# Performance work log

Measured on AMD Instinct MI355X. Metric: run time of the kernel, lower is better.

## Reference

```python
import jax, jax.numpy as jnp
import numpy as np

B = 131072
D = 64          # d_model
T = 4           # num_tiles
TEMP = 0.5


def setup_inputs() -> dict:
    key = jax.random.key(0)
    ks = jax.random.split(key, 16)
    s = 0.02
    return {
        "a_vec": jax.random.normal(ks[0], (B, D), dtype=jnp.float32),
        "b_vec": jax.random.normal(ks[1], (B, D), dtype=jnp.float32),
        "pos_encoding": jax.random.normal(ks[2], (B, 8), dtype=jnp.float32),
        # router: Linear(2D+8 -> D), GELU, Linear(D -> T)
        "Wr1": jax.random.normal(ks[3], (2 * D + 8, D), dtype=jnp.float32) * s,
        "br1": jnp.zeros((D,), dtype=jnp.float32),
        "Wr2": jax.random.normal(ks[4], (D, T), dtype=jnp.float32) * s,
        "br2": jnp.zeros((T,), dtype=jnp.float32),
        # tile nets: per-tile Linear(2D -> 2D), GELU, Linear(2D -> D)
        "W1": jax.random.normal(ks[5], (T, 2 * D, 2 * D), dtype=jnp.float32) * s,
        "b1": jnp.zeros((T, 2 * D), dtype=jnp.float32),
        "W2": jax.random.normal(ks[6], (T, 2 * D, D), dtype=jnp.float32) * s,
        "b2": jnp.zeros((T, D), dtype=jnp.float32),
    }


def _router(x, Wr1, br1, Wr2, br2):
    h = jax.nn.gelu(x @ Wr1 + br1, approximate=False)  # torch nn.GELU is exact
    return (h @ Wr2 + br2) / TEMP


def reference(a_vec, b_vec, pos_encoding, Wr1, br1, Wr2, br2, W1, b1, W2, b2):
    pair = jnp.concatenate([a_vec, b_vec], axis=-1)            # (B, 2D)

    # Routing 1 uses pair; routing 2 uses flipped pair. Both expert passes
    # consume `pair` (faithful to the original code, which feeds pair both times).
    idx1 = jnp.argmax(_router(jnp.concatenate([pair, pos_encoding], -1),
                              Wr1, br1, Wr2, br2), axis=-1)    # (B,)
    pair_flip = jnp.concatenate([b_vec, a_vec], axis=-1)
    idx2 = jnp.argmax(_router(jnp.concatenate([pair_flip, pos_encoding], -1),
                              Wr1, br1, Wr2, br2), axis=-1)    # (B,)

    # Run all tiles on every sample (small T), then gather the routed output.
    h = jax.nn.gelu(jnp.einsum('bi,tij->btj', pair, W1) + b1, approximate=False)  # (B,T,2D)
    out_all = jnp.einsum('bth,thd->btd', h, W2) + b2                              # (B,T,D)

    out1 = jnp.take_along_axis(out_all, idx1[:, None, None], axis=1)[:, 0]
    out2 = jnp.take_along_axis(out_all, idx2[:, None, None], axis=1)[:, 0]
    return out1, out2
```

## Files before the change

kernel.cpp:

```cpp
#include <hip/hip_runtime.h>

#define B_N 131072

using bfrag_t = __attribute__((ext_vector_type(8))) short;
using acc_t   = __attribute__((ext_vector_type(4))) float;
using v4f     = __attribute__((ext_vector_type(4))) float;
using i32x4_t = __attribute__((ext_vector_type(4))) int;

__device__ __forceinline__ unsigned short f2bf(float f) {
  unsigned int u = __float_as_uint(f);
  u += 0x7FFFu + ((u >> 16) & 1u);
  return (unsigned short)(u >> 16);
}

__device__ __forceinline__ unsigned int pk2bf(float x, float y) {
  return (unsigned int)f2bf(x) | ((unsigned int)f2bf(y) << 16);
}

__device__ __forceinline__ void gload_lds16(const void* g, void* l) {
  __builtin_amdgcn_global_load_lds((const __attribute__((address_space(1))) void*)g,
                                   (__attribute__((address_space(3))) void*)l, 16, 0, 0);
}

__device__ __forceinline__ float gelu_f(float x) {
  float ax = fabsf(x) * 0.70710678118654752f;
  float t  = __builtin_amdgcn_rcpf(fmaf(0.3275911f, ax, 1.0f));
  float p  = fmaf(1.061405429f, t, -1.453152027f);
  p = fmaf(p, t, 1.421413741f);
  p = fmaf(p, t, -0.284496736f);
  p = fmaf(p, t, 0.254829592f);
  p = p * t;
  float e  = __expf(-ax * ax);
  float er = fmaf(-p, e, 1.0f);
  er = (x < 0.0f) ? -er : er;
  return 0.5f * x * (1.0f + er);
}

__global__ __launch_bounds__(256) void prepack2_k(
    const float* __restrict__ Wr1, const float* __restrict__ br1,
    const float* __restrict__ Wr2, const float* __restrict__ br2,
    const float* __restrict__ W1, const float* __restrict__ W2,
    float* __restrict__ RW, short* __restrict__ W1s, short* __restrict__ W2s) {
  int gt = blockIdx.x * 256 + threadIdx.x;
  for (int idx = gt; idx < 142 * 64; idx += 16384) {
    int row = idx >> 6, j = idx & 63; float val;
    if (row < 136)      val = Wr1[row * 64 + j];
    else if (row == 136) val = br1[j];
    else if (row < 141) val = Wr2[(row - 137) * 64 + j];
    else                val = (j < 4) ? br2[j] : 0.0f;
    RW[idx] = val;
  }
  for (int ch = gt; ch < 8192; ch += 16384) {
    int t = ch >> 11, r = (ch >> 4) & 127, c = ch & 15;
    const float* src = W1 + t * 16384 + r;
    short* dst = W1s + (t * 128 + r) * 128 + ((c ^ (r & 15)) * 8);
    #pragma unroll
    for (int m = 0; m < 8; m++) dst[m] = (short)f2bf(src[(c * 8 + m) * 128]);
  }
  for (int ch = gt; ch < 4096; ch += 16384) {
    int t = ch >> 10, d = (ch >> 4) & 63, c = ch & 15;
    const float* src = W2 + t * 8192 + d;
    short* dst = W2s + (t * 64 + d) * 128 + ((c ^ (d & 15)) * 8);
    #pragma unroll
    for (int m = 0; m < 8; m++) dst[m] = (short)f2bf(src[(c * 8 + m) * 64]);
  }
}

__global__ __launch_bounds__(256) void router6_k(
    const float* __restrict__ a, const float* __restrict__ b,
    const float* __restrict__ pos, const float* __restrict__ RW,
    unsigned char* __restrict__ r1, unsigned char* __restrict__ r2) {
  __shared__ float SB[17928];
  const int XA = 9088, XB = 13248, PP = 17408;
  int tid = threadIdx.x, wave = tid >> 6, lane = tid & 63;
  int s0 = blockIdx.x * 64;

  for (int it = 0; it < 9; it++) {
    int cb = it * 256 + wave * 64;
    if (cb < 2272) {
      int chunk = cb + lane;
      if (chunk < 2272) gload_lds16(RW + chunk * 4, (char*)SB + cb * 16);
    }
  }
  #pragma unroll
  for (int it = 0; it < 4; it++) {
    int idx = it * 256 + tid;
    int s = idx >> 4, c = idx & 15;
    v4f va = *(const v4f*)(a + (size_t)(s0 + s) * 64 + c * 4);
    v4f vb = *(const v4f*)(b + (size_t)(s0 + s) * 64 + c * 4);
    #pragma unroll
    for (int k = 0; k < 4; k++) {
      SB[XA + (c * 4 + k) * 65 + s] = va[k];
      SB[XB + (c * 4 + k) * 65 + s] = vb[k];
    }
  }
  #pragma unroll
  for (int r = 0; r < 2; r++) {
    int idx = r * 256 + tid;
    int s = idx >> 3, c = idx & 7;
    SB[PP + c * 65 + s] = pos[(size_t)(s0 + s) * 8 + c];
  }
  __syncthreads();

  int sq = tid >> 2, jq = tid & 3;
  v4f acc1[4], acc2[4];
  #pragma unroll
  for (int e = 0; e < 4; e++) {
    v4f bi = *(const v4f*)(SB + 136 * 64 + jq * 16 + e * 4);
    acc1[e] = bi; acc2[e] = bi;
  }
  #pragma unroll 4
  for (int i = 0; i < 64; ++i) {
    float xa = SB[XA + i * 65 + sq];
    float xb = SB[XB + i * 65 + sq];
    const v4f* w = (const v4f*)(SB + i * 64 + jq * 16);
    v4f xav = {xa, xa, xa, xa}, xbv = {xb, xb, xb, xb};
    #pragma unroll
    for (int e = 0; e < 4; e++) {
      v4f wv = w[e];
      acc1[e] = __builtin_elementwise_fma(xav, wv, acc1[e]);
      acc2[e] = __builtin_elementwise_fma(xbv, wv, acc2[e]);
    }
  }
  #pragma unroll 4
  for (int i = 0; i < 64; ++i) {
    float xa = SB[XA + i * 65 + sq];
    float xb = SB[XB + i * 65 + sq];
    const v4f* w = (const v4f*)(SB + (64 + i) * 64 + jq * 16);
    v4f xav = {xa, xa, xa, xa}, xbv = {xb, xb, xb, xb};
    #pragma unroll
    for (int e = 0; e < 4; e++) {
      v4f wv = w[e];
      acc1[e] = __builtin_elementwise_fma(xbv, wv, acc1[e]);
      acc2[e] = __builtin_elementwise_fma(xav, wv, acc2[e]);
    }
  }
  #pragma unroll 2
  for (int i = 0; i < 8; ++i) {
    float p = SB[PP + i * 65 + sq];
    const v4f* w = (const v4f*)(SB + (128 + i) * 64 + jq * 16);
    v4f pv = {p, p, p, p};
    #pragma unroll
    for (int e = 0; e < 4; e++) {
      v4f wv = w[e];
      acc1[e] = __builtin_elementwise_fma(pv, wv, acc1[e]);
      acc2[e] = __builtin_elementwise_fma(pv, wv, acc2[e]);
    }
  }
  #pragma unroll
  for (int e = 0; e < 4; e++) {
    #pragma unroll
    for (int c = 0; c < 4; c++) {
      acc1[e][c] = gelu_f(acc1[e][c]);
      acc2[e][c] = gelu_f(acc2[e][c]);
    }
  }
  __syncthreads();
  #pragma unroll
  for (int e = 0; e < 4; e++) {
    #pragma unroll
    for (int c = 0; c < 4; c++) {
      int j = jq * 16 + e * 4 + c;
      SB[XA + j * 65 + sq] = acc1[e][c];
      SB[XB + j * 65 + sq] = acc2[e][c];
    }
  }
  __syncthreads();
  v4f l1 = *(const v4f*)(SB + 141 * 64);
  v4f l2 = l1;
  #pragma unroll 4
  for (int j = 0; j < 64; ++j) {
    float h1 = SB[XA + j * 65 + sq];
    float h2 = SB[XB + j * 65 + sq];
    v4f w2 = *(const v4f*)(SB + 137 * 64 + j * 4);
    v4f h1v = {h1, h1, h1, h1}, h2v = {h2, h2, h2, h2};
    l1 = __builtin_elementwise_fma(h1v, w2, l1);
    l2 = __builtin_elementwise_fma(h2v, w2, l2);
  }
  int idx1 = 0; float b1v = l1[0];
  if (l1[1] > b1v) { b1v = l1[1]; idx1 = 1; }
  if (l1[2] > b1v) { b1v = l1[2]; idx1 = 2; }
  if (l1[3] > b1v) { b1v = l1[3]; idx1 = 3; }
  int idx2 = 0; float b2v = l2[0];
  if (l2[1] > b2v) { b2v = l2[1]; idx2 = 1; }
  if (l2[2] > b2v) { b2v = l2[2]; idx2 = 2; }
  if (l2[3] > b2v) { b2v = l2[3]; idx2 = 3; }
  if (jq == 0) {
    r1[s0 + sq] = (unsigned char)idx1;
    r2[s0 + sq] = (unsigned char)idx2;
  }
}

__global__ __launch_bounds__(256) void expert2_k(
    const float* __restrict__ a, const float* __restrict__ b,
    const short* __restrict__ W1s, const short* __restrict__ W2s,
    const float* __restrict__ b1, const float* __restrict__ b2,
    const unsigned char* __restrict__ r1, const unsigned char* __restrict__ r2,
    float* __restrict__ out) {
  __shared__ short LB[24576];
  int tid = threadIdx.x;
  int wave = tid >> 6, lane = tid & 63;
  int q = lane >> 4, sm = lane & 15;
  int s0 = blockIdx.x * 128;

  #pragma unroll
  for (int r = 0; r < 8; r++) {
    int slot = r * 256 + tid;
    int g = slot >> 10, sg = slot & 1023;
    int f = sg >> 6, l = sg & 63;
    int sgrp = f >> 2, kb = f & 3;
    int s = s0 + g * 64 + sgrp * 16 + (l & 15);
    int k = kb * 32 + (l >> 4) * 8;
    const float* src = (k < 64) ? (a + s * 64 + k) : (b + s * 64 + (k - 64));
    acc_t v0 = *(const acc_t*)(src);
    acc_t v1 = *(const acc_t*)(src + 4);
    i32x4_t pk;
    pk[0] = (int)pk2bf(v0[0], v0[1]);
    pk[1] = (int)pk2bf(v0[2], v0[3]);
    pk[2] = (int)pk2bf(v1[0], v1[1]);
    pk[3] = (int)pk2bf(v1[2], v1[3]);
    *(i32x4_t*)(&LB[slot * 8]) = pk;
  }
  __syncthreads();
  bfrag_t bfrag[2][4];
  #pragma unroll
  for (int g = 0; g < 2; g++)
    #pragma unroll
    for (int kb = 0; kb < 4; kb++)
      bfrag[g][kb] = *(const bfrag_t*)(&LB[((g * 16 + wave * 4 + kb) * 64 + lane) * 8]);

  int sA = s0 + wave * 16 + sm, sB = sA + 64;
  int i1A = (int)r1[sA], i2A = (int)r2[sA];
  int i1B = (int)r1[sB], i2B = (int)r2[sB];
  __syncthreads();

  acc_t zero = {0.f, 0.f, 0.f, 0.f};
  acc_t o1[2][4], o2[2][4];
  #pragma unroll
  for (int g = 0; g < 2; g++)
    #pragma unroll
    for (int i = 0; i < 4; i++) { o1[g][i] = zero; o2[g][i] = zero; }

  int vb[4];
  #pragma unroll
  for (int kb = 0; kb < 4; kb++) vb[kb] = sm * 256 + (((kb * 4 + q) ^ sm) * 16);
  int addr0 = (((q & 1) * 2) * 16 + sm) * 4;
  int addr1 = addr0 + 64;
  bool hi = (q >> 1) != 0;

  for (int t = 0; t < 4; t++) {
    #pragma unroll
    for (int it = 0; it < 12; it++) {
      int cb = it * 256 + wave * 64;
      int chunk = cb + lane;
      const short* gsrc = (chunk < 2048) ? (W1s + t * 16384 + chunk * 8)
                                         : (W2s + t * 8192 + (chunk - 2048) * 8);
      gload_lds16(gsrc, (char*)LB + cb * 16);
    }
    __syncthreads();
    #pragma unroll
    for (int g = 0; g < 2; g++) {
      unsigned int hp[8][2];
      #pragma unroll
      for (int mt = 0; mt < 8; mt++) {
        acc_t c = zero;
        #pragma unroll
        for (int kb = 0; kb < 4; kb++) {
          bfrag_t A = *(const bfrag_t*)((const char*)LB + mt * 4096 + vb[kb]);
          c = __builtin_amdgcn_mfma_f32_16x16x32_bf16(A, bfrag[g][kb], c, 0, 0, 0);
        }
        acc_t bv = *(const acc_t*)(b1 + t * 128 + mt * 16 + q * 4);
        float g0 = gelu_f(c[0] + bv[0]);
        float g1 = gelu_f(c[1] + bv[1]);
        float g2 = gelu_f(c[2] + bv[2]);
        float g3 = gelu_f(c[3] + bv[3]);
        hp[mt][0] = pk2bf(g0, g1);
        hp[mt][1] = pk2bf(g2, g3);
      }
      bfrag_t b2f[4];
      #pragma unroll
      for (int kb2 = 0; kb2 < 4; kb2++) {
        int p00 = __builtin_amdgcn_ds_bpermute(addr0, (int)hp[2 * kb2][0]);
        int p01 = __builtin_amdgcn_ds_bpermute(addr0, (int)hp[2 * kb2][1]);
        int p10 = __builtin_amdgcn_ds_bpermute(addr1, (int)hp[2 * kb2][0]);
        int p11 = __builtin_amdgcn_ds_bpermute(addr1, (int)hp[2 * kb2][1]);
        int q00 = __builtin_amdgcn_ds_bpermute(addr0, (int)hp[2 * kb2 + 1][0]);
        int q01 = __builtin_amdgcn_ds_bpermute(addr0, (int)hp[2 * kb2 + 1][1]);
        int q10 = __builtin_amdgcn_ds_bpermute(addr1, (int)hp[2 * kb2 + 1][0]);
        int q11 = __builtin_amdgcn_ds_bpermute(addr1, (int)hp[2 * kb2 + 1][1]);
        i32x4_t w;
        w[0] = hi ? q00 : p00;
        w[1] = hi ? q01 : p01;
        w[2] = hi ? q10 : p10;
        w[3] = hi ? q11 : p11;
        b2f[kb2] = __builtin_bit_cast(bfrag_t, w);
      }
      int i1g = g ? i1B : i1A;
      int i2g = g ? i2B : i2A;
      #pragma unroll
      for (int mt2 = 0; mt2 < 4; mt2++) {
        acc_t c = zero;
        #pragma unroll
        for (int kb2 = 0; kb2 < 4; kb2++) {
          bfrag_t A = *(const bfrag_t*)((const char*)LB + 32768 + mt2 * 4096 + vb[kb2]);
          c = __builtin_amdgcn_mfma_f32_16x16x32_bf16(A, b2f[kb2], c, 0, 0, 0);
        }
        acc_t bv = *(const acc_t*)(b2 + t * 64 + mt2 * 16 + q * 4);
        c[0] += bv[0]; c[1] += bv[1]; c[2] += bv[2]; c[3] += bv[3];
        o1[g][mt2] = (i1g == t) ? c : o1[g][mt2];
        o2[g][mt2] = (i2g == t) ? c : o2[g][mt2];
      }
    }
    __syncthreads();
  }
  #pragma unroll
  for (int g = 0; g < 2; g++) {
    int so = g ? sB : sA;
    float* p1 = out + so * 64 + q * 4;
    float* p2 = out + (size_t)B_N * 64 + so * 64 + q * 4;
    #pragma unroll
    for (int mt2 = 0; mt2 < 4; mt2++) {
      *(acc_t*)(p1 + mt2 * 16) = o1[g][mt2];
      *(acc_t*)(p2 + mt2 * 16) = o2[g][mt2];
    }
  }
}

extern "C" void kernel_launch(void* const* d_in, const int* in_sizes, int n_in,
                              void* d_out, int out_size, void* d_ws, size_t ws_size,
                              hipStream_t stream) {
  const float* a   = (const float*)d_in[0];
  const float* bv  = (const float*)d_in[1];
  const float* pos = (const float*)d_in[2];
  const float* Wr1 = (const float*)d_in[3];
  const float* br1 = (const float*)d_in[4];
  const float* Wr2 = (const float*)d_in[5];
  const float* br2 = (const float*)d_in[6];
  const float* W1  = (const float*)d_in[7];
  const float* b1  = (const float*)d_in[8];
  const float* W2  = (const float*)d_in[9];
  const float* b2  = (const float*)d_in[10];
  float* out = (float*)d_out;

  unsigned char* r1 = (unsigned char*)d_ws;
  unsigned char* r2 = r1 + B_N;
  float* RW  = (float*)((char*)d_ws + 262144);
  short* W1s = (short*)((char*)d_ws + 298496);
  short* W2s = (short*)((char*)d_ws + 429568);

  prepack2_k<<<64, 256, 0, stream>>>(Wr1, br1, Wr2, br2, W1, W2, RW, W1s, W2s);
  router6_k<<<B_N / 64, 256, 0, stream>>>(a, bv, pos, RW, r1, r2);
  expert2_k<<<B_N / 128, 256, 0, stream>>>(a, bv, W1s, W2s, b1, b2, r1, r2, out);
}
```

Baseline: 271.6 us.

## Route samples to experts via sorted lists instead of computing all four tiles

Replaces the run-every-tile-then-select expert kernel with a grouped MoE dispatch. The router counts per-expert assignments, a single-block kernel computes padded offsets, and a placement kernel scatters (sample, slot) entries into per-expert lists. The expert kernel then processes 128 entries of one expert per block and writes results directly, doing roughly half the MLP work and loading weights once per block. The cost is two extra kernel launches, global atomics, gathered rather than contiguous input reads, scattered output writes, and nondeterministic list ordering.

```diff
diff --git a/kernel.cpp b/kernel.cpp
--- a/kernel.cpp
+++ b/kernel.cpp
@@ -40,8 +40,10 @@
     const float* __restrict__ Wr1, const float* __restrict__ br1,
     const float* __restrict__ Wr2, const float* __restrict__ br2,
     const float* __restrict__ W1, const float* __restrict__ W2,
-    float* __restrict__ RW, short* __restrict__ W1s, short* __restrict__ W2s) {
+    float* __restrict__ RW, short* __restrict__ W1s, short* __restrict__ W2s,
+    unsigned int* __restrict__ counts) {
   int gt = blockIdx.x * 256 + threadIdx.x;
+  if (gt < 4) counts[gt] = 0u;
   for (int idx = gt; idx < 142 * 64; idx += 16384) {
     int row = idx >> 6, j = idx & 63; float val;
     if (row < 136)      val = Wr1[row * 64 + j];
@@ -66,14 +68,17 @@
   }
 }
 
-__global__ __launch_bounds__(256) void router6_k(
+__global__ __launch_bounds__(256) void router7_k(
     const float* __restrict__ a, const float* __restrict__ b,
     const float* __restrict__ pos, const float* __restrict__ RW,
-    unsigned char* __restrict__ r1, unsigned char* __restrict__ r2) {
+    unsigned char* __restrict__ r1, unsigned char* __restrict__ r2,
+    unsigned int* __restrict__ gcounts) {
   __shared__ float SB[17928];
+  __shared__ unsigned int hcnt[4];
   const int XA = 9088, XB = 13248, PP = 17408;
   int tid = threadIdx.x, wave = tid >> 6, lane = tid & 63;
   int s0 = blockIdx.x * 64;
+  if (tid < 4) hcnt[tid] = 0u;
 
   for (int it = 0; it < 9; it++) {
     int cb = it * 256 + wave * 64;
@@ -188,20 +193,79 @@
   if (jq == 0) {
     r1[s0 + sq] = (unsigned char)idx1;
     r2[s0 + sq] = (unsigned char)idx2;
-  }
-}
-
-__global__ __launch_bounds__(256) void expert2_k(
+    atomicAdd(&hcnt[idx1], 1u);
+    atomicAdd(&hcnt[idx2], 1u);
+  }
+  __syncthreads();
+  if (tid < 4) atomicAdd(&gcounts[tid], hcnt[tid]);
+}
+
+__global__ __launch_bounds__(256) void offsets_k(
+    const unsigned int* __restrict__ counts, unsigned int* __restrict__ table,
+    unsigned int* __restrict__ cursors, unsigned int* __restrict__ list) {
+  __shared__ unsigned int ps[5], cnt[4];
+  int tid = threadIdx.x;
+  if (tid == 0) {
+    unsigned int acc = 0;
+    for (int t = 0; t < 4; t++) {
+      ps[t] = acc;
+      unsigned int c = counts[t];
+      cnt[t] = c;
+      acc += ((c + 127u) >> 7) << 7;
+    }
+    ps[4] = acc;
+    #pragma unroll
+    for (int t = 0; t < 5; t++) table[t] = ps[t];
+    #pragma unroll
+    for (int t = 0; t < 4; t++) cursors[t] = ps[t];
+  }
+  __syncthreads();
+  #pragma unroll
+  for (int r = 0; r < 2; r++) {
+    int idx = r * 256 + tid;
+    int t = idx >> 7, i = idx & 127;
+    unsigned int pos = ps[t] + cnt[t] + (unsigned int)i;
+    if (pos < ps[t + 1]) list[pos] = 0xFFFFFFFFu;
+  }
+}
+
+__global__ __launch_bounds__(256) void place_k(
+    const unsigned char* __restrict__ r1, const unsigned char* __restrict__ r2,
+    unsigned int* __restrict__ cursors, unsigned int* __restrict__ list) {
+  __shared__ unsigned int lc[4], lb[4];
+  int tid = threadIdx.x;
+  if (tid < 4) lc[tid] = 0u;
+  __syncthreads();
+  int s = blockIdx.x * 256 + tid;
+  int e1 = (int)r1[s], e2 = (int)r2[s];
+  unsigned int k1 = atomicAdd(&lc[e1], 1u);
+  unsigned int k2 = atomicAdd(&lc[e2], 1u);
+  __syncthreads();
+  if (tid < 4) lb[tid] = atomicAdd(&cursors[tid], lc[tid]);
+  __syncthreads();
+  list[lb[e1] + k1] = ((unsigned int)s << 1);
+  list[lb[e2] + k2] = ((unsigned int)s << 1) | 1u;
+}
+
+__global__ __launch_bounds__(256) void expert3_k(
     const float* __restrict__ a, const float* __restrict__ b,
     const short* __restrict__ W1s, const short* __restrict__ W2s,
     const float* __restrict__ b1, const float* __restrict__ b2,
-    const unsigned char* __restrict__ r1, const unsigned char* __restrict__ r2,
+    const unsigned int* __restrict__ table, const unsigned int* __restrict__ list,
     float* __restrict__ out) {
   __shared__ short LB[24576];
+  __shared__ unsigned int eLS[128];
   int tid = threadIdx.x;
   int wave = tid >> 6, lane = tid & 63;
   int q = lane >> 4, sm = lane & 15;
-  int s0 = blockIdx.x * 128;
+
+  unsigned int p0 = blockIdx.x * 128u;
+  unsigned int t1 = table[1], t2 = table[2], t3 = table[3], t4 = table[4];
+  if (p0 >= t4) return;
+  int t = (p0 >= t1) + (p0 >= t2) + (p0 >= t3);
+
+  if (tid < 128) eLS[tid] = list[p0 + tid];
+  __syncthreads();
 
   #pragma unroll
   for (int r = 0; r < 8; r++) {
@@ -209,9 +273,11 @@
     int g = slot >> 10, sg = slot & 1023;
     int f = sg >> 6, l = sg & 63;
     int sgrp = f >> 2, kb = f & 3;
-    int s = s0 + g * 64 + sgrp * 16 + (l & 15);
+    int ls2 = g * 64 + sgrp * 16 + (l & 15);
+    unsigned int e = eLS[ls2];
+    int s = (e == 0xFFFFFFFFu) ? 0 : (int)(e >> 1);
     int k = kb * 32 + (l >> 4) * 8;
-    const float* src = (k < 64) ? (a + s * 64 + k) : (b + s * 64 + (k - 64));
+    const float* src = (k < 64) ? (a + (size_t)s * 64 + k) : (b + (size_t)s * 64 + (k - 64));
     acc_t v0 = *(const acc_t*)(src);
     acc_t v1 = *(const acc_t*)(src + 4);
     i32x4_t pk;
@@ -229,18 +295,11 @@
     for (int kb = 0; kb < 4; kb++)
       bfrag[g][kb] = *(const bfrag_t*)(&LB[((g * 16 + wave * 4 + kb) * 64 + lane) * 8]);
 
-  int sA = s0 + wave * 16 + sm, sB = sA + 64;
-  int i1A = (int)r1[sA], i2A = (int)r2[sA];
-  int i1B = (int)r1[sB], i2B = (int)r2[sB];
+  unsigned int eA = eLS[wave * 16 + sm];
+  unsigned int eB = eLS[64 + wave * 16 + sm];
   __syncthreads();
 
   acc_t zero = {0.f, 0.f, 0.f, 0.f};
-  acc_t o1[2][4], o2[2][4];
-  #pragma unroll
-  for (int g = 0; g < 2; g++)
-    #pragma unroll
-    for (int i = 0; i < 4; i++) { o1[g][i] = zero; o2[g][i] = zero; }
-
   int vb[4];
   #pragma unroll
   for (int kb = 0; kb < 4; kb++) vb[kb] = sm * 256 + (((kb * 4 + q) ^ sm) * 16);
@@ -248,80 +307,68 @@
   int addr1 = addr0 + 64;
   bool hi = (q >> 1) != 0;
 
-  for (int t = 0; t < 4; t++) {
-    #pragma unroll
-    for (int it = 0; it < 12; it++) {
-      int cb = it * 256 + wave * 64;
-      int chunk = cb + lane;
-      const short* gsrc = (chunk < 2048) ? (W1s + t * 16384 + chunk * 8)
-                                         : (W2s + t * 8192 + (chunk - 2048) * 8);
-      gload_lds16(gsrc, (char*)LB + cb * 16);
-    }
-    __syncthreads();
-    #pragma unroll
-    for (int g = 0; g < 2; g++) {
-      unsigned int hp[8][2];
+  #pragma unroll
+  for (int it = 0; it < 12; it++) {
+    int cb = it * 256 + wave * 64;
+    int chunk = cb + lane;
+    const short* gsrc = (chunk < 2048) ? (W1s + t * 16384 + chunk * 8)
+                                       : (W2s + t * 8192 + (chunk - 2048) * 8);
+    gload_lds16(gsrc, (char*)LB + cb * 16);
+  }
+  __syncthreads();
+
+  #pragma unroll
+  for (int g = 0; g < 2; g++) {
+    unsigned int hp[8][2];
+    #pragma unroll
+    for (int mt = 0; mt < 8; mt++) {
+      acc_t c = zero;
       #pragma unroll
-      for (int mt = 0; mt < 8; mt++) {
-        acc_t c = zero;
-        #pragma unroll
-        for (int kb = 0; kb < 4; kb++) {
-          bfrag_t A = *(const bfrag_t*)((const char*)LB + mt * 4096 + vb[kb]);
-          c = __builtin_amdgcn_mfma_f32_16x16x32_bf16(A, bfrag[g][kb], c, 0, 0, 0);
-        }
-        acc_t bv = *(const acc_t*)(b1 + t * 128 + mt * 16 + q * 4);
-        float g0 = gelu_f(c[0] + bv[0]);
-        float g1 = gelu_f(c[1] + bv[1]);
-        float g2 = gelu_f(c[2] + bv[2]);
-        float g3 = gelu_f(c[3] + bv[3]);
-        hp[mt][0] = pk2bf(g0, g1);
-        hp[mt][1] = pk2bf(g2, g3);
+      for (int kb = 0; kb < 4; kb++) {
+        bfrag_t A = *(const bfrag_t*)((const char*)LB + mt * 4096 + vb[kb]);
+        c = __builtin_amdgcn_mfma_f32_16x16x32_bf16(A, bfrag[g][kb], c, 0, 0, 0);
       }
-      bfrag_t b2f[4];
+      acc_t bv = *(const acc_t*)(b1 + t * 128 + mt * 16 + q * 4);
+      float g0 = gelu_f(c[0] + bv[0]);
+      float g1 = gelu_f(c[1] + bv[1]);
+      float g2 = gelu_f(c[2] + bv[2]);
+      float g3 = gelu_f(c[3] + bv[3]);
+      hp[mt][0] = pk2bf(g0, g1);
+      hp[mt][1] = pk2bf(g2, g3);
+    }
+    bfrag_t b2f[4];
+    #pragma unroll
+    for (int kb2 = 0; kb2 < 4; kb2++) {
+      int p00 = __builtin_amdgcn_ds_bpermute(addr0, (int)hp[2 * kb2][0]);
+      int p01 = __builtin_amdgcn_ds_bpermute(addr0, (int)hp[2 * kb2][1]);
+      int p10 = __builtin_amdgcn_ds_bpermute(addr1, (int)hp[2 * kb2][0]);
+      int p11 = __builtin_amdgcn_ds_bpermute(addr1, (int)hp[2 * kb2][1]);
+      int q00 = __builtin_amdgcn_ds_bpermute(addr0, (int)hp[2 * kb2 + 1][0]);
+      int q01 = __builtin_amdgcn_ds_bpermute(addr0, (int)hp[2 * kb2 + 1][1]);
+      int q10 = __builtin_amdgcn_ds_bpermute(addr1, (int)hp[2 * kb2 + 1][0]);
+      int q11 = __builtin_amdgcn_ds_bpermute(addr1, (int)hp[2 * kb2 + 1][1]);
+      i32x4_t w;
+      w[0] = hi ? q00 : p00;
+      w[1] = hi ? q01 : p01;
+      w[2] = hi ? q10 : p10;
+      w[3] = hi ? q11 : p11;
+      b2f[kb2] = __builtin_bit_cast(bfrag_t, w);
+    }
+    unsigned int e = g ? eB : eA;
+    bool live = (e != 0xFFFFFFFFu);
+    size_t so = ((size_t)(e & 1u)) * B_N + (size_t)(e >> 1);
+    float* p = out + so * 64 + q * 4;
+    #pragma unroll
+    for (int mt2 = 0; mt2 < 4; mt2++) {
+      acc_t c = zero;
       #pragma unroll
       for (int kb2 = 0; kb2 < 4; kb2++) {
-        int p00 = __builtin_amdgcn_ds_bpermute(addr0, (int)hp[2 * kb2][0]);
-        int p01 = __builtin_amdgcn_ds_bpermute(addr0, (int)hp[2 * kb2][1]);
-        int p10 = __builtin_amdgcn_ds_bpermute(addr1, (int)hp[2 * kb2][0]);
-        int p11 = __builtin_amdgcn_ds_bpermute(addr1, (int)hp[2 * kb2][1]);
-        int q00 = __builtin_amdgcn_ds_bpermute(addr0, (int)hp[2 * kb2 + 1][0]);
-        int q01 = __builtin_amdgcn_ds_bpermute(addr0, (int)hp[2 * kb2 + 1][1]);
-        int q10 = __builtin_amdgcn_ds_bpermute(addr1, (int)hp[2 * kb2 + 1][0]);
-        int q11 = __builtin_amdgcn_ds_bpermute(addr1, (int)hp[2 * kb2 + 1][1]);
-        i32x4_t w;
-        w[0] = hi ? q00 : p00;
-        w[1] = hi ? q01 : p01;
-        w[2] = hi ? q10 : p10;
-        w[3] = hi ? q11 : p11;
-        b2f[kb2] = __builtin_bit_cast(bfrag_t, w);
+        bfrag_t A = *(const bfrag_t*)((const char*)LB + 32768 + mt2 * 4096 + vb[kb2]);
+        c = __builtin_amdgcn_mfma_f32_16x16x32_bf16(A, b2f[kb2], c, 0, 0, 0);
       }
-      int i1g = g ? i1B : i1A;
-      int i2g = g ? i2B : i2A;
-      #pragma unroll
-      for (int mt2 = 0; mt2 < 4; mt2++) {
-        acc_t c = zero;
-        #pragma unroll
-        for (int kb2 = 0; kb2 < 4; kb2++) {
-          bfrag_t A = *(const bfrag_t*)((const char*)LB + 32768 + mt2 * 4096 + vb[kb2]);
-          c = __builtin_amdgcn_mfma_f32_16x16x32_bf16(A, b2f[kb2], c, 0, 0, 0);
-        }
-        acc_t bv = *(const acc_t*)(b2 + t * 64 + mt2 * 16 + q * 4);
-        c[0] += bv[0]; c[1] += bv[1]; c[2] += bv[2]; c[3] += bv[3];
-        o1[g][mt2] = (i1g == t) ? c : o1[g][mt2];
-        o2[g][mt2] = (i2g == t) ? c : o2[g][mt2];
-      }
-    }
-    __syncthreads();
-  }
-  #pragma unroll
-  for (int g = 0; g < 2; g++) {
-    int so = g ? sB : sA;
-    float* p1 = out + so * 64 + q * 4;
-    float* p2 = out + (size_t)B_N * 64 + so * 64 + q * 4;
-    #pragma unroll
-    for (int mt2 = 0; mt2 < 4; mt2++) {
-      *(acc_t*)(p1 + mt2 * 16) = o1[g][mt2];
-      *(acc_t*)(p2 + mt2 * 16) = o2[g][mt2];
+      acc_t bv = *(const acc_t*)(b2 + t * 64 + mt2 * 16 + q * 4);
+      c[0] += bv[0]; c[1] += bv[1]; c[2] += bv[2]; c[3] += bv[3];
+      if (live) *(acc_t*)(p + mt2 * 16) = c;
     }
   }
 }
@@ -347,8 +394,14 @@
   float* RW  = (float*)((char*)d_ws + 262144);
   short* W1s = (short*)((char*)d_ws + 298496);
   short* W2s = (short*)((char*)d_ws + 429568);
-
-  prepack2_k<<<64, 256, 0, stream>>>(Wr1, br1, Wr2, br2, W1, W2, RW, W1s, W2s);
-  router6_k<<<B_N / 64, 256, 0, stream>>>(a, bv, pos, RW, r1, r2);
-  expert2_k<<<B_N / 128, 256, 0, stream>>>(a, bv, W1s, W2s, b1, b2, r1, r2, out);
-}
+  unsigned int* counts  = (unsigned int*)((char*)d_ws + 495104);
+  unsigned int* cursors = (unsigned int*)((char*)d_ws + 495120);
+  unsigned int* table   = (unsigned int*)((char*)d_ws + 495136);
+  unsigned int* list    = (unsigned int*)((char*)d_ws + 495168);
+
+  prepack2_k<<<64, 256, 0, stream>>>(Wr1, br1, Wr2, br2, W1, W2, RW, W1s, W2s, counts);
+  router7_k<<<B_N / 64, 256, 0, stream>>>(a, bv, pos, RW, r1, r2, counts);
+  offsets_k<<<1, 256, 0, stream>>>(counts, table, cursors, list);
+  place_k<<<B_N / 256, 256, 0, stream>>>(r1, r2, cursors, list);
+  expert3_k<<<2052, 256, 0, stream>>>(a, bv, W1s, W2s, b1, b2, table, list, out);
+}
```

Result: faster. 254.2 us (-6.4%).
